# Kernel tuning notes

Measured on AMD Instinct MI355X. Metric: run time of the kernel, lower is better.

Reference implementation:

```python
import jax, jax.numpy as jnp
import numpy as np

NH, NOPE_D, ROPE_D, V_D, R = 16, 48, 16, 64, 128
EPS = 1e-6

def rms_norm(x, w):
    norm = jax.lax.rsqrt(jnp.mean(jnp.square(x), axis=-1, keepdims=True) + EPS)
    return x * norm * w

def apply_rope(x, cos, sin):
    # x: (..., rope_d); cos/sin broadcastable (..., rope_d//2)
    d = x.shape[-1]
    x1, x2 = x[..., : d // 2], x[..., d // 2 :]
    return jnp.concatenate([x1 * cos - x2 * sin, x2 * cos + x1 * sin], axis=-1)

def setup_inputs() -> dict:
    key = jax.random.key(0)
    ks = jax.random.split(key, 8)
    B, T, D = 2, 2048, 1024
    s = lambda fan_in: 1.0 / np.sqrt(fan_in)
    return {
        "x": jax.random.normal(ks[0], (B, T, D), jnp.float32),
        "cos": jax.random.uniform(ks[1], (T, ROPE_D // 2), jnp.float32),
        "sin": jax.random.uniform(ks[2], (T, ROPE_D // 2), jnp.float32),
        "Wq": jax.random.normal(ks[3], (NH * (NOPE_D + ROPE_D), D), jnp.float32) * s(D),
        "q_norm_w": jnp.ones((NOPE_D + ROPE_D,), jnp.float32),
        "Wkva": jax.random.normal(ks[4], (R + ROPE_D, D), jnp.float32) * s(D),
        "kva_norm_w": jnp.ones((R,), jnp.float32),
        "Wkvb": jax.random.normal(ks[5], (NH * (NOPE_D + V_D), R), jnp.float32) * s(R),
        "Wo": jax.random.normal(ks[6], (D, NH * V_D), jnp.float32) * s(NH * V_D),
    }

def reference(x, cos, sin, Wq, q_norm_w, Wkva, kva_norm_w, Wkvb, Wo):
    B, T, D = x.shape
    # Q path: project, per-head RMSNorm over (nope+rope) dims, split
    q = (x @ Wq.T).reshape(B, T, NH, NOPE_D + ROPE_D)
    q = rms_norm(q, q_norm_w)
    q_nope, q_rope = q[..., :NOPE_D], q[..., NOPE_D:]
    # Low-rank KV path
    kv_a = x @ Wkva.T  # (B,T,R+ROPE_D)
    kv_latent = rms_norm(kv_a[..., :R], kva_norm_w)
    k_rope_raw = kv_a[..., R:]  # (B,T,ROPE_D) shared across heads
    kv_b = (kv_latent @ Wkvb.T).reshape(B, T, NH, NOPE_D + V_D)
    k_nope, v = kv_b[..., :NOPE_D], kv_b[..., NOPE_D:]
    # Decoupled RoPE
    cos_t = cos[None, :T, None, :]  # (1,T,1,rope_d/2)
    sin_t = sin[None, :T, None, :]
    q_rope = apply_rope(q_rope, cos_t, sin_t)
    k_rope = apply_rope(k_rope_raw[:, :, None, :], cos[None, :T, None, :], sin[None, :T, None, :])
    k_rope = jnp.broadcast_to(k_rope, (B, T, NH, ROPE_D))
    q_full = jnp.concatenate([q_nope, q_rope], axis=-1)  # (B,T,NH,64)
    k_full = jnp.concatenate([k_nope, k_rope], axis=-1)
    # Causal attention, scale = 1/sqrt(nope+rope)
    scale = (NOPE_D + ROPE_D) ** -0.5
    scores = jnp.einsum("bqhd,bkhd->bhqk", q_full, k_full) * scale
    causal = jnp.tril(jnp.ones((T, T), bool))
    scores = jnp.where(causal[None, None], scores, -jnp.inf)
    attn = jax.nn.softmax(scores, axis=-1)
    out = jnp.einsum("bhqk,bkhd->bqhd", attn, v).reshape(B, T, NH * V_D)
    return out @ Wo.T
```

## Files before the change

### kernel.cpp

```cpp
#include <hip/hip_runtime.h>
#include <hip/hip_bf16.h>
#include <math.h>

#define NH 16
#define T_ 2048
#define B_ 2
#define D_ 1024
#define EPS 1e-6f

typedef __attribute__((ext_vector_type(8))) short bf16x8;
typedef __attribute__((ext_vector_type(4))) short bf16x4;
typedef __attribute__((ext_vector_type(4))) float f32x4;

__device__ __forceinline__ float wred_sum(float v){
  #pragma unroll
  for (int o = 32; o > 0; o >>= 1) v += __shfl_xor(v, o, 64);
  return v;
}

__device__ __forceinline__ unsigned pack_bf16(float a, float b){
  __hip_bfloat162 t = __float22bfloat162_rn(make_float2(a, b));
  unsigned r; __builtin_memcpy(&r, &t, 4); return r;
}

__device__ __forceinline__ void gload_lds16(const void* g, void* l){
  __builtin_amdgcn_global_load_lds((const __attribute__((address_space(1))) void*)g,
                                   (__attribute__((address_space(3))) void*)l, 16, 0, 0);
}

__device__ __forceinline__ f32x4 mfma16(bf16x4 a, bf16x4 b, f32x4 c){
#if __has_builtin(__builtin_amdgcn_mfma_f32_16x16x16bf16_1k)
  return __builtin_amdgcn_mfma_f32_16x16x16bf16_1k(a, b, c, 0, 0, 0);
#else
  asm volatile("v_mfma_f32_16x16x16_bf16 %0, %1, %2, %0" : "+v"(c) : "v"(a), "v"(b));
  return c;
#endif
}

__global__ __launch_bounds__(256)
void cvt5(const float* __restrict__ x, const float* __restrict__ wq,
          const float* __restrict__ wkva, const float* __restrict__ wkvb,
          const float* __restrict__ wo,
          __hip_bfloat16* __restrict__ xb, __hip_bfloat16* __restrict__ wqb,
          __hip_bfloat16* __restrict__ wkvab, __hip_bfloat16* __restrict__ wkvbb,
          __hip_bfloat16* __restrict__ wob)
{
  const int i = blockIdx.x * 256 + threadIdx.x;
  const float* s; __hip_bfloat16* d; size_t soff, doff;
  if      (i < 1048576) { s = x;    d = xb;    soff = doff = i; }
  else if (i < 1310720) { s = wq;   d = wqb;   soff = doff = i - 1048576; }
  else if (i < 1347584) { s = wkva; d = wkvab; soff = doff = i - 1310720; }
  else if (i < 1404928) {
    const int off = i - 1347584;
    const int srow = off >> 5, c4 = off & 31;
    const int h = srow / 112, dd = srow % 112;
    const int drow = (dd < 48) ? (h*48 + dd) : (768 + h*64 + (dd - 48));
    s = wkvb; d = wkvbb; soff = off; doff = (size_t)drow*32 + c4;
  }
  else                  { s = wo;   d = wob;   soff = doff = i - 1404928; }
  float4 v = *(const float4*)(s + soff * 4);
  *(__hip_bfloat162*)(d + doff * 4)     = __float22bfloat162_rn(make_float2(v.x, v.y));
  *(__hip_bfloat162*)(d + doff * 4 + 2) = __float22bfloat162_rn(make_float2(v.z, v.w));
}

template<typename CT>
__global__ __launch_bounds__(256, 2)
void gemm_bt64(const __hip_bfloat16* __restrict__ A, const __hip_bfloat16* __restrict__ W,
               CT* __restrict__ C, int M, int N, int K)
{
  __shared__ __hip_bfloat16 As[2][128 * 64];
  __shared__ __hip_bfloat16 Ws[2][64 * 64];
  const int tid = threadIdx.x;
  const int wv = tid >> 6, lane = tid & 63;
  const int m = lane & 15, quad = lane >> 4;
  const int bm = blockIdx.y * 128, bn = blockIdx.x * 64;

  const __hip_bfloat16* ga[4];
  const __hip_bfloat16* gw[2];
  #pragma unroll
  for (int i = 0; i < 4; i++) {
    const int slot = i*256 + tid;
    const int row = slot >> 3, cb = slot & 7;
    ga[i] = A + (size_t)(bm + row) * K + ((cb ^ (row & 7)) << 3);
  }
  #pragma unroll
  for (int i = 0; i < 2; i++) {
    const int slot = i*256 + tid;
    const int row = slot >> 3, cb = slot & 7;
    int wr = bn + row; if (wr >= N) wr = N - 1;
    gw[i] = W + (size_t)wr * K + ((cb ^ (row & 7)) << 3);
  }
  auto stage = [&](int buf){
    #pragma unroll
    for (int i = 0; i < 4; i++) { gload_lds16(ga[i], &As[buf][(i*256 + wv*64)*8]); ga[i] += 64; }
    #pragma unroll
    for (int i = 0; i < 2; i++) { gload_lds16(gw[i], &Ws[buf][(i*256 + wv*64)*8]); gw[i] += 64; }
  };

  f32x4 acc[2][4];
  #pragma unroll
  for (int mi = 0; mi < 2; mi++)
    #pragma unroll
    for (int nj = 0; nj < 4; nj++) acc[mi][nj] = (f32x4){0.f,0.f,0.f,0.f};

  stage(0);
  const int iters = K >> 6;
  for (int it = 0; it < iters; it++) {
    const int cur = it & 1;
    __syncthreads();
    if (it + 1 < iters) stage(cur ^ 1);
    #pragma unroll
    for (int ks = 0; ks < 2; ks++) {
      const int cb = ((ks*4 + quad) ^ (m & 7)) << 3;
      bf16x8 af[2], wf[4];
      #pragma unroll
      for (int mi = 0; mi < 2; mi++)
        af[mi] = *(const bf16x8*)(&As[cur][(wv*32 + mi*16 + m) * 64 + cb]);
      #pragma unroll
      for (int nj = 0; nj < 4; nj++)
        wf[nj] = *(const bf16x8*)(&Ws[cur][(nj*16 + m) * 64 + cb]);
      #pragma unroll
      for (int mi = 0; mi < 2; mi++)
        #pragma unroll
        for (int nj = 0; nj < 4; nj++)
          acc[mi][nj] = __builtin_amdgcn_mfma_f32_16x16x32_bf16(af[mi], wf[nj], acc[mi][nj], 0, 0, 0);
    }
  }

  #pragma unroll
  for (int mi = 0; mi < 2; mi++)
    #pragma unroll
    for (int nj = 0; nj < 4; nj++) {
      const int col = bn + nj*16 + m;
      if (col < N) {
        #pragma unroll
        for (int r = 0; r < 4; r++) {
          const int row = bm + wv*32 + mi*16 + quad*4 + r;
          if constexpr (sizeof(CT) == 2)
            C[(size_t)row * N + col] = (CT)__float2bfloat16(acc[mi][nj][r]);
          else
            C[(size_t)row * N + col] = acc[mi][nj][r];
        }
      }
    }
}

__global__ __launch_bounds__(256, 2)
void gemm_qkva(const __hip_bfloat16* __restrict__ A, const __hip_bfloat16* __restrict__ Wqb,
               const __hip_bfloat16* __restrict__ Wkvab,
               const float* __restrict__ qw, const float* __restrict__ cosp,
               const float* __restrict__ sinp,
               __hip_bfloat16* __restrict__ qb, float* __restrict__ kva)
{
  __shared__ __hip_bfloat16 As[2][128 * 64];
  __shared__ __hip_bfloat16 Ws[2][64 * 64];
  const int K = 1024;
  const int tid = threadIdx.x;
  const int wv = tid >> 6, lane = tid & 63;
  const int m = lane & 15, quad = lane >> 4;
  const int bm = blockIdx.y * 128;
  const bool isq = blockIdx.x < 16;
  const __hip_bfloat16* W = isq ? Wqb : Wkvab;
  const int bn = isq ? blockIdx.x*64 : (blockIdx.x - 16)*64;
  const int Nw = isq ? 1024 : 144;

  const __hip_bfloat16* ga[4];
  const __hip_bfloat16* gw[2];
  #pragma unroll
  for (int i = 0; i < 4; i++) {
    const int slot = i*256 + tid;
    const int row = slot >> 3, cb = slot & 7;
    ga[i] = A + (size_t)(bm + row) * K + ((cb ^ (row & 7)) << 3);
  }
  #pragma unroll
  for (int i = 0; i < 2; i++) {
    const int slot = i*256 + tid;
    const int row = slot >> 3, cb = slot & 7;
    int wr = bn + row; if (wr >= Nw) wr = Nw - 1;
    gw[i] = W + (size_t)wr * K + ((cb ^ (row & 7)) << 3);
  }
  auto stage = [&](int buf){
    #pragma unroll
    for (int i = 0; i < 4; i++) { gload_lds16(ga[i], &As[buf][(i*256 + wv*64)*8]); ga[i] += 64; }
    #pragma unroll
    for (int i = 0; i < 2; i++) { gload_lds16(gw[i], &Ws[buf][(i*256 + wv*64)*8]); gw[i] += 64; }
  };

  f32x4 acc[2][4];
  #pragma unroll
  for (int mi = 0; mi < 2; mi++)
    #pragma unroll
    for (int nj = 0; nj < 4; nj++) acc[mi][nj] = (f32x4){0.f,0.f,0.f,0.f};

  stage(0);
  for (int it = 0; it < 16; it++) {
    const int cur = it & 1;
    __syncthreads();
    if (it < 15) stage(cur ^ 1);
    #pragma unroll
    for (int ks = 0; ks < 2; ks++) {
      const int cb = ((ks*4 + quad) ^ (m & 7)) << 3;
      bf16x8 af[2], wf[4];
      #pragma unroll
      for (int mi = 0; mi < 2; mi++)
        af[mi] = *(const bf16x8*)(&As[cur][(wv*32 + mi*16 + m) * 64 + cb]);
      #pragma unroll
      for (int nj = 0; nj < 4; nj++)
        wf[nj] = *(const bf16x8*)(&Ws[cur][(nj*16 + m) * 64 + cb]);
      #pragma unroll
      for (int mi = 0; mi < 2; mi++)
        #pragma unroll
        for (int nj = 0; nj < 4; nj++)
          acc[mi][nj] = __builtin_amdgcn_mfma_f32_16x16x32_bf16(af[mi], wf[nj], acc[mi][nj], 0, 0, 0);
    }
  }

  if (isq) {
    const int head = blockIdx.x;
    float qwv[4];
    #pragma unroll
    for (int nj = 0; nj < 4; nj++) qwv[nj] = qw[nj*16 + m];
    const int j = m & 7;
    const float qscale = 0.125f * 1.44269504f;
    #pragma unroll
    for (int mi = 0; mi < 2; mi++) {
      #pragma unroll
      for (int r = 0; r < 4; r++) {
        float ss = 0.f;
        #pragma unroll
        for (int nj = 0; nj < 4; nj++) { const float t = acc[mi][nj][r]; ss = fmaf(t, t, ss); }
        ss += __shfl_xor(ss, 1, 64); ss += __shfl_xor(ss, 2, 64);
        ss += __shfl_xor(ss, 4, 64); ss += __shfl_xor(ss, 8, 64);
        const float nrm = rsqrtf(ss * (1.0f/64.0f) + EPS);
        float v[4];
        #pragma unroll
        for (int nj = 0; nj < 4; nj++) v[nj] = acc[mi][nj][r] * nrm * qwv[nj];
        const int grow = bm + wv*32 + mi*16 + quad*4 + r;
        const int t = grow & (T_ - 1);
        const int b = grow >> 11;
        const float part = __shfl_xor(v[3], 8, 64);
        const float c = cosp[t*8 + j], sn = sinp[t*8 + j];
        v[3] = (m < 8) ? (v[3]*c - part*sn) : (v[3]*c + part*sn);
        __hip_bfloat16* dst = qb + ((size_t)(b*NH + head)*T_ + t)*64 + m;
        #pragma unroll
        for (int nj = 0; nj < 4; nj++) dst[nj*16] = __float2bfloat16(v[nj] * qscale);
      }
    }
  } else {
    #pragma unroll
    for (int mi = 0; mi < 2; mi++)
      #pragma unroll
      for (int nj = 0; nj < 4; nj++) {
        const int col = bn + nj*16 + m;
        if (col < 144) {
          #pragma unroll
          for (int r = 0; r < 4; r++) {
            const int row = bm + wv*32 + mi*16 + quad*4 + r;
            kva[(size_t)row * 144 + col] = acc[mi][nj][r];
          }
        }
      }
  }
}

__global__ void prep_kv(const float* __restrict__ kva, const float* __restrict__ kw,
                        const float* __restrict__ cosp, const float* __restrict__ sinp,
                        __hip_bfloat16* __restrict__ kvl16, __hip_bfloat16* __restrict__ krope16)
{
  const int tid = threadIdx.x;
  const int bt = blockIdx.x;
  const int t = bt % T_;
  const float* row = kva + (size_t)bt * 144;
  const float v = row[tid];
  float s = wred_sum(v * v);
  __shared__ float red[2];
  if ((tid & 63) == 0) red[tid >> 6] = s;
  __syncthreads();
  const float total = red[0] + red[1];
  const float norm = rsqrtf(total * (1.0f/128.0f) + EPS);
  kvl16[(size_t)bt * 128 + tid] = __float2bfloat16(v * norm * kw[tid]);
  if (tid < 16) {
    const int j = tid & 7;
    const float c = cosp[t*8 + j], sn = sinp[t*8 + j];
    const float x1 = row[128 + j], x2 = row[136 + j];
    krope16[(size_t)bt * 16 + tid] = __float2bfloat16((tid < 8) ? (x1 * c - x2 * sn)
                                                               : (x2 * c + x1 * sn));
  }
}

__global__ __launch_bounds__(256, 2)
void gemm_kvb(const __hip_bfloat16* __restrict__ A, const __hip_bfloat16* __restrict__ W,
              __hip_bfloat16* __restrict__ knope, __hip_bfloat16* __restrict__ vt)
{
  __shared__ __hip_bfloat16 As[2][128 * 64];
  __shared__ __hip_bfloat16 Ws[2][64 * 64];
  const int K = 128;
  const int tid = threadIdx.x;
  const int wv = tid >> 6, lane = tid & 63;
  const int m = lane & 15, quad = lane >> 4;
  const int bm = blockIdx.y * 128, bn = blockIdx.x * 64;

  const __hip_bfloat16* ga[4];
  const __hip_bfloat16* gw[2];
  #pragma unroll
  for (int i = 0; i < 4; i++) {
    const int slot = i*256 + tid;
    const int row = slot >> 3, cb = slot & 7;
    ga[i] = A + (size_t)(bm + row) * K + ((cb ^ (row & 7)) << 3);
  }
  #pragma unroll
  for (int i = 0; i < 2; i++) {
    const int slot = i*256 + tid;
    const int row = slot >> 3, cb = slot & 7;
    gw[i] = W + (size_t)(bn + row) * K + ((cb ^ (row & 7)) << 3);
  }
  auto stage = [&](int buf){
    #pragma unroll
    for (int i = 0; i < 4; i++) { gload_lds16(ga[i], &As[buf][(i*256 + wv*64)*8]); ga[i] += 64; }
    #pragma unroll
    for (int i = 0; i < 2; i++) { gload_lds16(gw[i], &Ws[buf][(i*256 + wv*64)*8]); gw[i] += 64; }
  };

  f32x4 acc[2][4];
  #pragma unroll
  for (int mi = 0; mi < 2; mi++)
    #pragma unroll
    for (int nj = 0; nj < 4; nj++) acc[mi][nj] = (f32x4){0.f,0.f,0.f,0.f};

  stage(0);
  for (int it = 0; it < 2; it++) {
    const int cur = it & 1;
    __syncthreads();
    if (it == 0) stage(1);
    #pragma unroll
    for (int ks = 0; ks < 2; ks++) {
      const int cb = ((ks*4 + quad) ^ (m & 7)) << 3;
      bf16x8 af[2], wf[4];
      #pragma unroll
      for (int mi = 0; mi < 2; mi++)
        af[mi] = *(const bf16x8*)(&As[cur][(wv*32 + mi*16 + m) * 64 + cb]);
      #pragma unroll
      for (int nj = 0; nj < 4; nj++)
        wf[nj] = *(const bf16x8*)(&Ws[cur][(nj*16 + m) * 64 + cb]);
      #pragma unroll
      for (int mi = 0; mi < 2; mi++)
        #pragma unroll
        for (int nj = 0; nj < 4; nj++)
          acc[mi][nj] = __builtin_amdgcn_mfma_f32_16x16x32_bf16(af[mi], wf[nj], acc[mi][nj], 0, 0, 0);
    }
  }

  if (bn < 768) {
    #pragma unroll
    for (int mi = 0; mi < 2; mi++)
      #pragma unroll
      for (int nj = 0; nj < 4; nj++) {
        const int col = bn + nj*16 + m;
        #pragma unroll
        for (int r = 0; r < 4; r++) {
          const int row = bm + wv*32 + mi*16 + quad*4 + r;
          knope[(size_t)row * 768 + col] = __float2bfloat16(acc[mi][nj][r]);
        }
      }
  } else {
    __syncthreads();
    short* TL = (short*)&As[0][0];
    #pragma unroll
    for (int mi = 0; mi < 2; mi++)
      #pragma unroll
      for (int nj = 0; nj < 4; nj++) {
        const int d = nj*16 + m;
        #pragma unroll
        for (int r = 0; r < 4; r++) {
          const int tl = wv*32 + mi*16 + quad*4 + r;
          __hip_bfloat16 hv = __float2bfloat16(acc[mi][nj][r]);
          short sv; __builtin_memcpy(&sv, &hv, 2);
          TL[d*136 + tl] = sv;
        }
      }
    __syncthreads();
    const int h = (bn - 768) >> 6;
    const int b = bm >> 11;
    const int t0 = bm & (T_ - 1);
    #pragma unroll
    for (int i = 0; i < 4; i++) {
      const int unit = i*256 + tid;
      const int d = unit >> 4, tu = unit & 15;
      *(bf16x8*)(vt + ((size_t)(b*NH + h)*64 + d)*T_ + t0 + tu*8)
          = *(const bf16x8*)(TL + d*136 + tu*8);
    }
  }
}

__device__ __forceinline__ void fa_store_t(float lrun, f32x4 (&o)[4],
    const int b, const int qbase, const int h, const int m, const int quad,
    __hip_bfloat16* __restrict__ aout)
{
  lrun += __shfl_xor(lrun, 16, 64);
  lrun += __shfl_xor(lrun, 32, 64);
  const float inv = 1.0f / lrun;
  const size_t base = (size_t)(b*T_ + qbase + m) * 1024 + h*64 + quad*4;
  #pragma unroll
  for (int vs = 0; vs < 4; vs++) {
    union { unsigned ui[2]; bf16x4 v; } pk;
    pk.ui[0] = pack_bf16(o[vs][0] * inv, o[vs][1] * inv);
    pk.ui[1] = pack_bf16(o[vs][2] * inv, o[vs][3] * inv);
    *(bf16x4*)(aout + base + vs*16) = pk.v;
  }
}

__global__ __launch_bounds__(256, 4)
void attn_tile(const __hip_bfloat16* __restrict__ qb,
               const __hip_bfloat16* __restrict__ knope,
               const __hip_bfloat16* __restrict__ krope16,
               const __hip_bfloat16* __restrict__ vt16,
               __hip_bfloat16* __restrict__ aout)
{
  __shared__ __hip_bfloat16 SL[16384];
  const int tid = threadIdx.x;
  const int wv = tid >> 6, lane = tid & 63;
  const int m = lane & 15, quad = lane >> 4;
  const int idx = (blockIdx.x + blockIdx.y) & 31;
  const int pj = idx & 7, pk = idx >> 3;
  const int qt = (pk == 0) ? pj : (pk == 1) ? (15 - pj) : (pk == 2) ? (16 + pj) : (31 - pj);
  const int bh = blockIdx.y;
  const int b = bh >> 4, h = bh & 15;
  const int qbase = qt*64 + wv*16;
  const int nt = qt + 1;

  const __hip_bfloat16* qr = qb + ((size_t)bh*T_ + qbase + m)*64 + quad*8;
  const bf16x8 q0 = *(const bf16x8*)qr, q1 = *(const bf16x8*)(qr + 32);

  const __hip_bfloat16* pK[2]; size_t iK[2];
  const __hip_bfloat16* pV[2];
  #pragma unroll
  for (int i = 0; i < 2; i++) {
    const int slot = i*256 + tid;
    const int krow = slot >> 3;
    const int kde = (slot & 7) ^ (krow & 7);
    if (kde < 6) { pK[i] = knope + (size_t)(b*T_ + krow)*768 + h*48 + kde*8; iK[i] = (size_t)64*768; }
    else         { pK[i] = krope16 + (size_t)(b*T_ + krow)*16 + (kde-6)*8;   iK[i] = (size_t)64*16; }
    pV[i] = vt16 + ((size_t)bh*64 + krow)*T_ + kde*8;
  }

  auto stage = [&](int buf){
    #pragma unroll
    for (int i = 0; i < 2; i++) {
      gload_lds16(pK[i], SL + buf*4096 + (i*256 + wv*64)*8);
      gload_lds16(pV[i], SL + 8192 + buf*4096 + (i*256 + wv*64)*8);
      pK[i] += iK[i]; pV[i] += 64;
    }
  };

  f32x4 o[4];
  #pragma unroll
  for (int vs = 0; vs < 4; vs++) o[vs] = (f32x4){0.f,0.f,0.f,0.f};
  float lrun = 0.f;

  const int sw0 = quad ^ (m & 7);
  const int qh = quad >> 1, ql = quad & 1;
  stage(0);

  for (int kt = 0; kt < nt; kt++) {
    const int cur = kt & 1;
    __syncthreads();
    if (kt + 1 < nt) stage(cur ^ 1);
    const __hip_bfloat16* Kc = SL + cur*4096;
    const __hip_bfloat16* Vc = SL + 8192 + cur*4096;
    const bool dtile = (kt == qt);

    f32x4 s[4];
    __builtin_amdgcn_s_setprio(1);
    #pragma unroll
    for (int sub = 0; sub < 4; sub++) {
      if (!dtile || sub <= wv) {
        const bf16x8 kf0 = *(const bf16x8*)(Kc + (sub*16 + m)*64 + sw0*8);
        const bf16x8 kf1 = *(const bf16x8*)(Kc + (sub*16 + m)*64 + (sw0^4)*8);
        f32x4 z = (f32x4){0.f,0.f,0.f,0.f};
        z = __builtin_amdgcn_mfma_f32_16x16x32_bf16(kf0, q0, z, 0, 0, 0);
        z = __builtin_amdgcn_mfma_f32_16x16x32_bf16(kf1, q1, z, 0, 0, 0);
        s[sub] = z;
      } else {
        s[sub] = (f32x4){-1e30f,-1e30f,-1e30f,-1e30f};
      }
    }
    __builtin_amdgcn_s_setprio(0);

    if (dtile) {
      #pragma unroll
      for (int sub = 0; sub < 4; sub++) {
        if (sub == wv) {
          #pragma unroll
          for (int r = 0; r < 4; r++)
            if (quad*4 + r > m) s[sub][r] = -1e30f;
        }
      }
    }

    bf16x4 u[4];
    #pragma unroll
    for (int sub = 0; sub < 4; sub++) {
      float p0 = exp2f(s[sub][0] - 48.0f), p1 = exp2f(s[sub][1] - 48.0f);
      float p2 = exp2f(s[sub][2] - 48.0f), p3 = exp2f(s[sub][3] - 48.0f);
      lrun += (p0 + p1) + (p2 + p3);
      union { unsigned ui[2]; bf16x4 v; } uu;
      uu.ui[0] = pack_bf16(p0, p1);
      uu.ui[1] = pack_bf16(p2, p3);
      u[sub] = uu.v;
    }

    __builtin_amdgcn_s_setprio(1);
    #pragma unroll
    for (int vs = 0; vs < 4; vs++) {
      #pragma unroll
      for (int sub = 0; sub < 4; sub++) {
        if (!dtile || sub <= wv) {
          const bf16x4 vf = *(const bf16x4*)(Vc + (vs*16 + m)*64
                              + (((sub*2 + qh) ^ (m & 7)) << 3) + (ql << 2));
          o[vs] = mfma16(vf, u[sub], o[vs]);
        }
      }
    }
    __builtin_amdgcn_s_setprio(0);
  }

  fa_store_t(lrun, o, b, qbase, h, m, quad, aout);
}

extern "C" void kernel_launch(void* const* d_in, const int* in_sizes, int n_in,
                              void* d_out, int out_size, void* d_ws, size_t ws_size,
                              hipStream_t stream)
{
  const float* x    = (const float*)d_in[0];
  const float* cosp = (const float*)d_in[1];
  const float* sinp = (const float*)d_in[2];
  const float* Wq   = (const float*)d_in[3];
  const float* qw   = (const float*)d_in[4];
  const float* Wkva = (const float*)d_in[5];
  const float* kw   = (const float*)d_in[6];
  const float* Wkvb = (const float*)d_in[7];
  const float* Wo   = (const float*)d_in[8];
  float* out = (float*)d_out;

  float* kva = (float*)d_ws;
  __hip_bfloat16* xb16    = (__hip_bfloat16*)(kva + 589824);
  __hip_bfloat16* knope16 = xb16 + 4194304;
  __hip_bfloat16* kvl16   = knope16 + 3145728;
  __hip_bfloat16* qb16    = kvl16 + 524288;
  __hip_bfloat16* vt16    = qb16 + 4194304;
  __hip_bfloat16* krope16 = vt16 + 4194304;
  __hip_bfloat16* Wqb     = krope16 + 65536;
  __hip_bfloat16* Wkvab   = Wqb + 1048576;
  __hip_bfloat16* Wkvbb   = Wkvab + 147456;
  __hip_bfloat16* Wob     = Wkvbb + 229376;
  __hip_bfloat16* ab16    = Wob + 1048576;

  const int M = B_ * T_;

  cvt5<<<6512, 256, 0, stream>>>(x, Wq, Wkva, Wkvb, Wo, xb16, Wqb, Wkvab, Wkvbb, Wob);
  gemm_qkva<<<dim3(19, 32), 256, 0, stream>>>(xb16, Wqb, Wkvab, qw, cosp, sinp, qb16, kva);
  prep_kv<<<M, 128, 0, stream>>>(kva, kw, cosp, sinp, kvl16, krope16);
  gemm_kvb<<<dim3(28, 32), 256, 0, stream>>>(kvl16, Wkvbb, knope16, vt16);
  attn_tile<<<dim3(32, B_ * NH), 256, 0, stream>>>(qb16, knope16, krope16, vt16, ab16);
  gemm_bt64<float><<<dim3(16, 32), 256, 0, stream>>>(ab16, Wob, out, M, 1024, 1024);
}
```

Baseline: 178.7 us.

## Split attention warps 2x2 over query and key halves with LDS reduction

Reorganizes the four waves of the attention tile from one 16-row query strip each into a 2x2 grid: each wave handles 32 query rows against half of the 64 keys. Each K and V fragment read from LDS is then reused for two query sub-tiles, which halves LDS fragment traffic per MFMA. The partial outputs and row sums of the two key-half waves are combined through shared memory after the loop. This adds a final cross-wave reduction, a barrier, and more accumulator registers per wave, which may lower occupancy under the launch bound.

```diff
diff --git a/kernel.cpp b/kernel.cpp
--- a/kernel.cpp
+++ b/kernel.cpp
@@ -392,23 +392,6 @@
   }
 }
 
-__device__ __forceinline__ void fa_store_t(float lrun, f32x4 (&o)[4],
-    const int b, const int qbase, const int h, const int m, const int quad,
-    __hip_bfloat16* __restrict__ aout)
-{
-  lrun += __shfl_xor(lrun, 16, 64);
-  lrun += __shfl_xor(lrun, 32, 64);
-  const float inv = 1.0f / lrun;
-  const size_t base = (size_t)(b*T_ + qbase + m) * 1024 + h*64 + quad*4;
-  #pragma unroll
-  for (int vs = 0; vs < 4; vs++) {
-    union { unsigned ui[2]; bf16x4 v; } pk;
-    pk.ui[0] = pack_bf16(o[vs][0] * inv, o[vs][1] * inv);
-    pk.ui[1] = pack_bf16(o[vs][2] * inv, o[vs][3] * inv);
-    *(bf16x4*)(aout + base + vs*16) = pk.v;
-  }
-}
-
 __global__ __launch_bounds__(256, 4)
 void attn_tile(const __hip_bfloat16* __restrict__ qb,
                const __hip_bfloat16* __restrict__ knope,
@@ -420,16 +403,20 @@
   const int tid = threadIdx.x;
   const int wv = tid >> 6, lane = tid & 63;
   const int m = lane & 15, quad = lane >> 4;
+  const int wq = wv >> 1, wk = wv & 1;
   const int idx = (blockIdx.x + blockIdx.y) & 31;
   const int pj = idx & 7, pk = idx >> 3;
   const int qt = (pk == 0) ? pj : (pk == 1) ? (15 - pj) : (pk == 2) ? (16 + pj) : (31 - pj);
   const int bh = blockIdx.y;
   const int b = bh >> 4, h = bh & 15;
-  const int qbase = qt*64 + wv*16;
   const int nt = qt + 1;
 
-  const __hip_bfloat16* qr = qb + ((size_t)bh*T_ + qbase + m)*64 + quad*8;
-  const bf16x8 q0 = *(const bf16x8*)qr, q1 = *(const bf16x8*)(qr + 32);
+  bf16x8 q0[2], q1[2];
+  #pragma unroll
+  for (int t2 = 0; t2 < 2; t2++) {
+    const __hip_bfloat16* qr = qb + ((size_t)bh*T_ + qt*64 + wq*32 + t2*16 + m)*64 + quad*8;
+    q0[t2] = *(const bf16x8*)qr; q1[t2] = *(const bf16x8*)(qr + 32);
+  }
 
   const __hip_bfloat16* pK[2]; size_t iK[2];
   const __hip_bfloat16* pV[2];
@@ -452,12 +439,14 @@
     }
   };
 
-  f32x4 o[4];
-  #pragma unroll
-  for (int vs = 0; vs < 4; vs++) o[vs] = (f32x4){0.f,0.f,0.f,0.f};
-  float lrun = 0.f;
-
-  const int sw0 = quad ^ (m & 7);
+  f32x4 o[2][4];
+  #pragma unroll
+  for (int t2 = 0; t2 < 2; t2++)
+    #pragma unroll
+    for (int vs = 0; vs < 4; vs++) o[t2][vs] = (f32x4){0.f,0.f,0.f,0.f};
+  float lrun[2] = {0.f, 0.f};
+
+  const int swk = quad ^ (m & 7);
   const int qh = quad >> 1, ql = quad & 1;
   stage(0);
 
@@ -469,62 +458,119 @@
     const __hip_bfloat16* Vc = SL + 8192 + cur*4096;
     const bool dtile = (kt == qt);
 
-    f32x4 s[4];
+    f32x4 s[2][2];
     __builtin_amdgcn_s_setprio(1);
     #pragma unroll
-    for (int sub = 0; sub < 4; sub++) {
-      if (!dtile || sub <= wv) {
-        const bf16x8 kf0 = *(const bf16x8*)(Kc + (sub*16 + m)*64 + sw0*8);
-        const bf16x8 kf1 = *(const bf16x8*)(Kc + (sub*16 + m)*64 + (sw0^4)*8);
-        f32x4 z = (f32x4){0.f,0.f,0.f,0.f};
-        z = __builtin_amdgcn_mfma_f32_16x16x32_bf16(kf0, q0, z, 0, 0, 0);
-        z = __builtin_amdgcn_mfma_f32_16x16x32_bf16(kf1, q1, z, 0, 0, 0);
-        s[sub] = z;
+    for (int ks = 0; ks < 2; ks++) {
+      const int gk2 = 2*wk + ks;
+      if (!dtile || gk2 <= 2*wq + 1) {
+        const __hip_bfloat16* kr = Kc + (wk*32 + ks*16 + m)*64;
+        const bf16x8 kf0 = *(const bf16x8*)(kr + swk*8);
+        const bf16x8 kf1 = *(const bf16x8*)(kr + (swk^4)*8);
+        #pragma unroll
+        for (int t2 = 0; t2 < 2; t2++) {
+          if (!dtile || gk2 <= 2*wq + t2) {
+            f32x4 z = (f32x4){0.f,0.f,0.f,0.f};
+            z = __builtin_amdgcn_mfma_f32_16x16x32_bf16(kf0, q0[t2], z, 0, 0, 0);
+            z = __builtin_amdgcn_mfma_f32_16x16x32_bf16(kf1, q1[t2], z, 0, 0, 0);
+            s[t2][ks] = z;
+          } else {
+            s[t2][ks] = (f32x4){-1e30f,-1e30f,-1e30f,-1e30f};
+          }
+        }
       } else {
-        s[sub] = (f32x4){-1e30f,-1e30f,-1e30f,-1e30f};
+        s[0][ks] = (f32x4){-1e30f,-1e30f,-1e30f,-1e30f};
+        s[1][ks] = (f32x4){-1e30f,-1e30f,-1e30f,-1e30f};
       }
     }
     __builtin_amdgcn_s_setprio(0);
 
     if (dtile) {
       #pragma unroll
-      for (int sub = 0; sub < 4; sub++) {
-        if (sub == wv) {
+      for (int ks = 0; ks < 2; ks++)
+        #pragma unroll
+        for (int t2 = 0; t2 < 2; t2++)
+          if (2*wk + ks == 2*wq + t2) {
+            #pragma unroll
+            for (int r = 0; r < 4; r++)
+              if (quad*4 + r > m) s[t2][ks][r] = -1e30f;
+          }
+    }
+
+    bf16x4 u[2][2];
+    #pragma unroll
+    for (int t2 = 0; t2 < 2; t2++)
+      #pragma unroll
+      for (int ks = 0; ks < 2; ks++) {
+        float p0 = exp2f(s[t2][ks][0] - 48.0f), p1 = exp2f(s[t2][ks][1] - 48.0f);
+        float p2 = exp2f(s[t2][ks][2] - 48.0f), p3 = exp2f(s[t2][ks][3] - 48.0f);
+        lrun[t2] += (p0 + p1) + (p2 + p3);
+        union { unsigned ui[2]; bf16x4 v; } uu;
+        uu.ui[0] = pack_bf16(p0, p1);
+        uu.ui[1] = pack_bf16(p2, p3);
+        u[t2][ks] = uu.v;
+      }
+
+    __builtin_amdgcn_s_setprio(1);
+    #pragma unroll
+    for (int vs = 0; vs < 4; vs++) {
+      #pragma unroll
+      for (int ks = 0; ks < 2; ks++) {
+        const int gk2 = 2*wk + ks;
+        if (!dtile || gk2 <= 2*wq + 1) {
+          const bf16x4 vf = *(const bf16x4*)(Vc + (vs*16 + m)*64
+                              + (((wk*4 + ks*2 + qh) ^ (m & 7)) << 3) + (ql << 2));
           #pragma unroll
-          for (int r = 0; r < 4; r++)
-            if (quad*4 + r > m) s[sub][r] = -1e30f;
+          for (int t2 = 0; t2 < 2; t2++)
+            if (!dtile || gk2 <= 2*wq + t2)
+              o[t2][vs] = mfma16(vf, u[t2][ks], o[t2][vs]);
         }
       }
     }
-
-    bf16x4 u[4];
-    #pragma unroll
-    for (int sub = 0; sub < 4; sub++) {
-      float p0 = exp2f(s[sub][0] - 48.0f), p1 = exp2f(s[sub][1] - 48.0f);
-      float p2 = exp2f(s[sub][2] - 48.0f), p3 = exp2f(s[sub][3] - 48.0f);
-      lrun += (p0 + p1) + (p2 + p3);
-      union { unsigned ui[2]; bf16x4 v; } uu;
-      uu.ui[0] = pack_bf16(p0, p1);
-      uu.ui[1] = pack_bf16(p2, p3);
-      u[sub] = uu.v;
-    }
-
-    __builtin_amdgcn_s_setprio(1);
-    #pragma unroll
-    for (int vs = 0; vs < 4; vs++) {
-      #pragma unroll
-      for (int sub = 0; sub < 4; sub++) {
-        if (!dtile || sub <= wv) {
-          const bf16x4 vf = *(const bf16x4*)(Vc + (vs*16 + m)*64
-                              + (((sub*2 + qh) ^ (m & 7)) << 3) + (ql << 2));
-          o[vs] = mfma16(vf, u[sub], o[vs]);
-        }
-      }
-    }
     __builtin_amdgcn_s_setprio(0);
   }
 
-  fa_store_t(lrun, o, b, qbase, h, m, quad, aout);
+  __syncthreads();
+  float* FB = (float*)SL;
+  float* LB = ((float*)SL) + 4096;
+  if (wk == 1) {
+    #pragma unroll
+    for (int t2 = 0; t2 < 2; t2++)
+      #pragma unroll
+      for (int vs = 0; vs < 4; vs++)
+        #pragma unroll
+        for (int r = 0; r < 4; r++)
+          FB[wq*2048 + ((t2*4 + vs)*4 + r)*64 + lane] = o[t2][vs][r];
+    LB[wq*128 + lane]      = lrun[0];
+    LB[wq*128 + 64 + lane] = lrun[1];
+  }
+  __syncthreads();
+  if (wk == 0) {
+    #pragma unroll
+    for (int t2 = 0; t2 < 2; t2++)
+      #pragma unroll
+      for (int vs = 0; vs < 4; vs++)
+        #pragma unroll
+        for (int r = 0; r < 4; r++)
+          o[t2][vs][r] += FB[wq*2048 + ((t2*4 + vs)*4 + r)*64 + lane];
+    lrun[0] += LB[wq*128 + lane];
+    lrun[1] += LB[wq*128 + 64 + lane];
+    #pragma unroll
+    for (int t2 = 0; t2 < 2; t2++) {
+      float l = lrun[t2];
+      l += __shfl_xor(l, 16, 64);
+      l += __shfl_xor(l, 32, 64);
+      const float inv = 1.0f / l;
+      const size_t base = (size_t)(b*T_ + qt*64 + wq*32 + t2*16 + m) * 1024 + h*64 + quad*4;
+      #pragma unroll
+      for (int vs = 0; vs < 4; vs++) {
+        union { unsigned ui[2]; bf16x4 v; } pkv;
+        pkv.ui[0] = pack_bf16(o[t2][vs][0] * inv, o[t2][vs][1] * inv);
+        pkv.ui[1] = pack_bf16(o[t2][vs][2] * inv, o[t2][vs][3] * inv);
+        *(bf16x4*)(aout + base + vs*16) = pkv.v;
+      }
+    }
+  }
 }
 
 extern "C" void kernel_launch(void* const* d_in, const int* in_sizes, int n_in,
```

Measured after the change: 177.0 us. No clear change (-1.0%).
